# Kernel optimization log

Measured on AMD Instinct MI355X. Metric: run time of the kernel, lower is better.

The kernel has to match this reference:

```python
import jax, jax.numpy as jnp
import numpy as np

BETA = 0.25


def setup_inputs() -> dict:
    key = jax.random.key(0)
    k1, k2 = jax.random.split(key)
    x = jax.random.normal(k1, (8, 256, 2048), dtype=jnp.float32)        # (B, C, L)
    codebook = jax.random.normal(k2, (8192, 256), dtype=jnp.float32)    # (K, C)
    return {"x": x, "codebook": codebook}


def reference(x, codebook):
    # x: (B, C, L) -> xt: (B, L, C)
    xt = jnp.transpose(x, (0, 2, 1))
    # Euclidean distances via ||a||^2 + ||b||^2 - 2 a.b (matches torch.cdist p=2)
    x_sq = jnp.sum(xt * xt, axis=-1, keepdims=True)          # (B, L, 1)
    c_sq = jnp.sum(codebook * codebook, axis=-1)             # (K,)
    dots = jnp.einsum('blc,kc->blk', xt, codebook)           # (B, L, K)
    dists = jnp.sqrt(jnp.maximum(x_sq + c_sq[None, None, :] - 2.0 * dots, 0.0))
    # NOTE: original code uses argmax over distances (faithfully reproduced)
    code = jnp.argmax(dists, axis=2)                         # (B, L) int
    emb = jnp.transpose(codebook[code], (0, 2, 1))           # (B, C, L)
    sg = jax.lax.stop_gradient
    loss = jnp.mean((sg(x) - emb) ** 2 + BETA * (sg(emb) - emb) ** 2)
    return code, emb, loss
```

## Files before the change

kernel.cpp:

```cpp
#include <hip/hip_runtime.h>
#include <hip/hip_fp16.h>
#include <stdint.h>

typedef unsigned int u32;
typedef unsigned long long u64;
typedef unsigned short ushort_t;

#define B_ 8
#define C_ 256
#define L_ 2048
#define K_ 8192
#define M_ 16384

#define WS_KEYS   0
#define WS_CNT    131072
#define WS_MAXCS  131076
#define WS_LOSS   131080
#define WS_XSQ    131328
#define WS_CSQ    196864
#define WS_LIST   295168
#define WS_LMAX   4489472
#define WS_XTH    12878080
#define WS_CBH    21266688
#define LIST_CAP  1048576u

typedef __attribute__((ext_vector_type(8))) short s8v;
typedef __attribute__((ext_vector_type(4))) float f4v;

__device__ __forceinline__ ushort_t f2bf(float f) {
  u32 u = __float_as_uint(f);
  u32 r = (u + 0x7FFFu + ((u >> 16) & 1u)) >> 16;
  return (ushort_t)r;
}

__device__ __forceinline__ void gld16(void* lds, const void* g) {
  __builtin_amdgcn_global_load_lds(
      (const __attribute__((address_space(1))) u32*)g,
      (__attribute__((address_space(3))) u32*)lds, 16, 0, 0);
}


__global__ void __launch_bounds__(256)
vq_transpose(const float* __restrict__ x, float* __restrict__ xtf,
             ushort_t* __restrict__ xth) {
  __shared__ float t[64][65];
  int tid = threadIdx.x;
  int b  = blockIdx.x >> 7;
  int cc = (blockIdx.x >> 5) & 3;
  int lc = blockIdx.x & 31;
#pragma unroll
  for (int j = 0; j < 4; ++j) {
    int c  = (tid >> 4) + j * 16;
    int lq = tid & 15;
    float4 v = *(const float4*)&x[((size_t)(b * C_ + cc * 64 + c)) * L_ + lc * 64 + lq * 4];
    t[c][lq * 4 + 0] = v.x; t[c][lq * 4 + 1] = v.y;
    t[c][lq * 4 + 2] = v.z; t[c][lq * 4 + 3] = v.w;
  }
  __syncthreads();
  int l = tid >> 2, qc = tid & 3;
  size_t m = (size_t)b * L_ + lc * 64 + l;
#pragma unroll
  for (int j = 0; j < 4; ++j) {
    int q = qc + j * 4;
    float4 v = make_float4(t[q * 4 + 0][l], t[q * 4 + 1][l],
                           t[q * 4 + 2][l], t[q * 4 + 3][l]);
    *(float4*)&xtf[m * C_ + cc * 64 + q * 4] = v;
    ushort4 h;
    h.x = f2bf(v.x); h.y = f2bf(v.y); h.z = f2bf(v.z); h.w = f2bf(v.w);
    *(ushort4*)&xth[m * C_ + cc * 64 + q * 4] = h;
  }
}

__global__ void vq_xsqt(const float* __restrict__ xtf, float* __restrict__ xsq) {
  int t = threadIdx.x;
  int m = blockIdx.x * 16 + (t >> 4);
  int g = t & 15;
  const float* row = xtf + (size_t)m * C_;
  float s = 0.0f;
#pragma unroll
  for (int j = 0; j < 4; ++j) {
    float4 v = *(const float4*)&row[g * 4 + j * 64];
    s += v.x * v.x + v.y * v.y + v.z * v.z + v.w * v.w;
  }
#pragma unroll
  for (int off = 1; off < 16; off <<= 1) s += __shfl_xor(s, off, 64);
  if (g == 0) xsq[m] = s;
}

__global__ void vq_cbprep(const float* __restrict__ cb, float* __restrict__ csq,
                          int* __restrict__ maxcs, ushort_t* __restrict__ cbh) {
  int t = threadIdx.x;
  int k = blockIdx.x * 16 + (t >> 4);
  int g = t & 15;
  const float* row = cb + (size_t)k * C_;
  float s = 0.0f;
#pragma unroll
  for (int j = 0; j < 4; ++j) {
    float4 v = *(const float4*)&row[g * 4 + j * 64];
    s += v.x * v.x + v.y * v.y + v.z * v.z + v.w * v.w;
    ushort4 h;
    h.x = f2bf(v.x); h.y = f2bf(v.y); h.z = f2bf(v.z); h.w = f2bf(v.w);
    *(ushort4*)&cbh[(size_t)k * C_ + g * 4 + j * 64] = h;
  }
#pragma unroll
  for (int off = 1; off < 16; off <<= 1) s += __shfl_xor(s, off, 64);
  if (g == 0) {
    csq[k] = s;
    atomicMax(maxcs, __float_as_int(s));
  }
}


#define STAGE(buf, t_)                                                        \
  {                                                                           \
    _Pragma("unroll")                                                         \
    for (int q = 0; q < 8; ++q) {                                             \
      int codeT = (w * 8 + q) * 2 + (l >> 5);                                 \
      int chunk = l & 31;                                                     \
      gld16(&Bs[(buf)][(w * 8 + q) * 512],                                    \
            &cbh[(size_t)(n0 + (t_) * 128 + codeT) * 256 +                    \
                 ((chunk ^ (codeT & 7)) * 8)]);                               \
    }                                                                         \
  }

__global__ void __launch_bounds__(512, 2)
vq_gemm(const ushort_t* __restrict__ xth, const ushort_t* __restrict__ cbh,
        const float* __restrict__ csq, __half* __restrict__ lmax) {
  __shared__ short Bs[2][128 * 256];

  const int tid = threadIdx.x;
  const int w = tid >> 6, l = tid & 63;
  const int lr = l & 15, lk = l >> 4;
  const int strip = blockIdx.x >> 2, ns = blockIdx.x & 3;
  const int r0 = strip * 256 + w * 32;
  const int n0 = ns * 2048;

  s8v a[2][8];
#pragma unroll
  for (int i = 0; i < 2; ++i)
#pragma unroll
    for (int ks = 0; ks < 8; ++ks)
      a[i][ks] = *(const s8v*)&xth[(size_t)(r0 + i * 16 + lr) * 256 + ks * 32 + lk * 8];

  STAGE(0, 0);
  __syncthreads();

  for (int t = 0; t < 16; ++t) {
    const int buf = t & 1;
    if (t < 15) STAGE(buf ^ 1, t + 1);

    f4v acc[2][8];
#pragma unroll
    for (int i = 0; i < 2; ++i)
#pragma unroll
      for (int j = 0; j < 8; ++j) acc[i][j] = (f4v){0.f, 0.f, 0.f, 0.f};

#pragma unroll
    for (int ks = 0; ks < 8; ++ks) {
      s8v b[8];
#pragma unroll
      for (int j = 0; j < 8; ++j) {
        int jrow = j * 16 + lr;
        b[j] = *(const s8v*)&Bs[buf][jrow * 256 + (((ks * 4 + lk) ^ (lr & 7)) * 8)];
      }
#pragma unroll
      for (int i = 0; i < 2; ++i)
#pragma unroll
        for (int j = 0; j < 8; ++j)
          acc[i][j] = __builtin_amdgcn_mfma_f32_16x16x32_bf16(a[i][ks], b[j], acc[i][j], 0, 0, 0);
    }

    float cq[8];
#pragma unroll
    for (int j = 0; j < 8; ++j) cq[j] = csq[n0 + t * 128 + j * 16 + lr];
#pragma unroll
    for (int i = 0; i < 2; ++i)
#pragma unroll
      for (int r = 0; r < 4; ++r) {
        float vb[4];
#pragma unroll
        for (int b2 = 0; b2 < 4; ++b2) {
          float v0 = __fmaf_rn(-2.0f, acc[i][2 * b2][r], cq[2 * b2]);
          float v1 = __fmaf_rn(-2.0f, acc[i][2 * b2 + 1][r], cq[2 * b2 + 1]);
          vb[b2] = fmaxf(v0, v1);
        }
#pragma unroll
        for (int off = 1; off < 16; off <<= 1)
#pragma unroll
          for (int b2 = 0; b2 < 4; ++b2)
            vb[b2] = fmaxf(vb[b2], __shfl_xor(vb[b2], off, 64));
        if (lr == 0) {
          short4 sv;
          sv.x = (short)__half_as_ushort(__float2half(vb[0]));
          sv.y = (short)__half_as_ushort(__float2half(vb[1]));
          sv.z = (short)__half_as_ushort(__float2half(vb[2]));
          sv.w = (short)__half_as_ushort(__float2half(vb[3]));
          *(short4*)&lmax[(size_t)(r0 + i * 16 + lk * 4 + r) * 256 + ns * 64 + t * 4] = sv;
        }
      }
    __syncthreads();
  }
}

__global__ void __launch_bounds__(256)
vq_thr(const __half* __restrict__ lmax, const float* __restrict__ xsq,
       const int* __restrict__ maxcs, u32* __restrict__ list, u32* __restrict__ cnt) {
  __shared__ u32 wcnt[4];
  __shared__ u32 gbase_s;
  const int t = threadIdx.x, w = t >> 6, l = t & 63;
  const int m0 = blockIdx.x * 64 + w * 16;
  const float mc = __int_as_float(*maxcs);

  ushort4 hv[16];
  float thv[16];
  u32 wtot = 0;
#pragma unroll
  for (int i = 0; i < 16; ++i) {
    int m = m0 + i;
    hv[i] = *(const ushort4*)&lmax[(size_t)m * 256 + l * 4];
    float v0 = __half2float(__ushort_as_half(hv[i].x));
    float v1 = __half2float(__ushort_as_half(hv[i].y));
    float v2 = __half2float(__ushort_as_half(hv[i].z));
    float v3 = __half2float(__ushort_as_half(hv[i].w));
    float g = fmaxf(fmaxf(v0, v1), fmaxf(v2, v3));
#pragma unroll
    for (int off = 1; off < 64; off <<= 1) g = fmaxf(g, __shfl_xor(g, off, 64));
    float th = g - (0.033f * sqrtf(xsq[m] * mc) + 0.6f);
    thv[i] = th;
    wtot += __popcll(__ballot(v0 >= th));
    wtot += __popcll(__ballot(v1 >= th));
    wtot += __popcll(__ballot(v2 >= th));
    wtot += __popcll(__ballot(v3 >= th));
  }
  if (l == 0) wcnt[w] = wtot;
  __syncthreads();
  if (t == 0) gbase_s = atomicAdd(cnt, wcnt[0] + wcnt[1] + wcnt[2] + wcnt[3]);
  __syncthreads();
  u32 off = gbase_s;
  for (int ww = 0; ww < w; ++ww) off += wcnt[ww];
#pragma unroll
  for (int i = 0; i < 16; ++i) {
    int m = m0 + i;
    float th = thv[i];
    float v[4];
    v[0] = __half2float(__ushort_as_half(hv[i].x));
    v[1] = __half2float(__ushort_as_half(hv[i].y));
    v[2] = __half2float(__ushort_as_half(hv[i].z));
    v[3] = __half2float(__ushort_as_half(hv[i].w));
#pragma unroll
    for (int j = 0; j < 4; ++j) {
      u64 mask = __ballot(v[j] >= th);
      if (v[j] >= th) {
        u32 pos = off + (u32)__popcll(mask & ((1ull << l) - 1ull));
        if (pos < LIST_CAP) list[pos] = ((u32)m << 8) | (u32)(l * 4 + j);
      }
      off += (u32)__popcll(mask);
    }
  }
}

__global__ void __launch_bounds__(256)
vq_rescore(const u32* __restrict__ list, const u32* __restrict__ cnt,
           const float* __restrict__ xtf, const float* __restrict__ cb,
           const float* __restrict__ xsq, const float* __restrict__ csq,
           u64* __restrict__ keys) {
  u32 n = *cnt; if (n > LIST_CAP) n = LIST_CAP;
  const int l = threadIdx.x & 63;
  const int u = l & 7;
  const int g = l >> 3;
  int wid = (blockIdx.x * 256 + threadIdx.x) >> 6;
  int nw = (gridDim.x * 256) >> 6;
  for (u32 e = wid; e < n; e += nw) {
    u32 ent = list[e];
    int m = (int)(ent >> 8), blk = (int)(ent & 255u);
    float4 xv[8];
#pragma unroll
    for (int i = 0; i < 8; ++i)
      xv[i] = *(const float4*)&xtf[(size_t)m * C_ + (i * 8 + u) * 4];
    float xq = xsq[m];
    u64 bestkey = 0;
#pragma unroll
    for (int cc = 0; cc < 4; ++cc) {
      int k = blk * 32 + cc * 8 + g;
      const float* crow = &cb[(size_t)k * C_];
      float p = 0.0f;
#pragma unroll
      for (int i = 0; i < 8; ++i) {
        float4 cv = *(const float4*)&crow[(i * 8 + u) * 4];
        p += xv[i].x * cv.x + xv[i].y * cv.y + xv[i].z * cv.z + xv[i].w * cv.w;
      }
#pragma unroll
      for (int off = 1; off < 8; off <<= 1) p += __shfl_xor(p, off, 64);
      if (u == 0) {
        float d2 = __fsub_rn(__fadd_rn(xq, csq[k]), __fmul_rn(2.0f, p));
        float dist = sqrtf(fmaxf(d2, 0.0f));
        u64 key = ((u64)__float_as_uint(dist) << 32) |
                  (u64)(0xFFFFFFFFu - (u32)k);
        if (key > bestkey) bestkey = key;
      }
    }
#pragma unroll
    for (int off = 8; off < 64; off <<= 1) {
      u64 o = __shfl_xor(bestkey, off, 64);
      if (o > bestkey) bestkey = o;
    }
    if (l == 0) atomicMax(&keys[m], bestkey);
  }
}


__global__ void vq_code(const u64* __restrict__ keys, float* __restrict__ out) {
  int m = blockIdx.x * 256 + threadIdx.x;
  u32 k = 0xFFFFFFFFu - (u32)(keys[m] & 0xFFFFFFFFull);
  out[m] = (float)k;
}

__global__ void __launch_bounds__(256)
vq_gather(const u64* __restrict__ keys, const float* __restrict__ cb,
          const float* __restrict__ x, float* __restrict__ emb,
          float* __restrict__ loss_acc) {
  __shared__ float rows[32 * 260];
  __shared__ int codes_s[32];
  __shared__ float partial[4];
  int t = threadIdx.x;
  int b = blockIdx.x >> 6;
  int l0 = (blockIdx.x & 63) * 32;
  if (t < 32) {
    u64 key = keys[b * L_ + l0 + t];
    codes_s[t] = (int)(0xFFFFFFFFu - (u32)(key & 0xFFFFFFFFull));
  }
  __syncthreads();
  {
    int r = t >> 3, c4 = t & 7;
    const float* src = cb + (size_t)codes_s[r] * C_;
#pragma unroll
    for (int j = 0; j < 8; ++j) {
      float4 v = *(const float4*)&src[(c4 + 8 * j) * 4];
      *(float4*)&rows[r * 260 + (c4 + 8 * j) * 4] = v;
    }
  }
  __syncthreads();
  float ls = 0.0f;
  int l = t & 31, cg = t >> 5;
#pragma unroll 4
  for (int cs = 0; cs < 32; ++cs) {
    int c = cg * 32 + cs;
    float v = rows[l * 260 + c];
    size_t gi = (size_t)(b * C_ + c) * L_ + l0 + l;
    emb[gi] = v;
    float d = x[gi] - v;
    ls = fmaf(d, d, ls);
  }
#pragma unroll
  for (int off = 1; off < 64; off <<= 1) ls += __shfl_xor(ls, off, 64);
  if ((t & 63) == 0) partial[t >> 6] = ls;
  __syncthreads();
  if (t == 0)
    atomicAdd(loss_acc, partial[0] + partial[1] + partial[2] + partial[3]);
}

__global__ void vq_loss(const float* __restrict__ loss_acc, float* __restrict__ out) {
  out[0] = loss_acc[0] / 4194304.0f;
}

extern "C" void kernel_launch(void* const* d_in, const int* in_sizes, int n_in,
                              void* d_out, int out_size, void* d_ws, size_t ws_size,
                              hipStream_t stream) {
  const float* x  = (const float*)d_in[0];
  const float* cb = (const float*)d_in[1];
  float* out = (float*)d_out;
  char* ws = (char*)d_ws;

  u64* keys      = (u64*)(ws + WS_KEYS);
  u32* cnt       = (u32*)(ws + WS_CNT);
  int* maxcs     = (int*)(ws + WS_MAXCS);
  float* loss_a  = (float*)(ws + WS_LOSS);
  float* xsq     = (float*)(ws + WS_XSQ);
  float* csq     = (float*)(ws + WS_CSQ);
  u32* list      = (u32*)(ws + WS_LIST);
  __half* lmax   = (__half*)(ws + WS_LMAX);
  ushort_t* xth  = (ushort_t*)(ws + WS_XTH);
  ushort_t* cbh  = (ushort_t*)(ws + WS_CBH);
  float* xtf     = out + M_;

  hipMemsetAsync(ws, 0, 131084, stream);

  vq_transpose<<<1024, 256, 0, stream>>>(x, xtf, xth);
  vq_cbprep<<<K_ / 16, 256, 0, stream>>>(cb, csq, maxcs, cbh);
  vq_xsqt<<<M_ / 16, 256, 0, stream>>>(xtf, xsq);
  vq_gemm<<<256, 512, 0, stream>>>(xth, cbh, csq, lmax);
  vq_thr<<<256, 256, 0, stream>>>(lmax, xsq, maxcs, list, cnt);
  vq_rescore<<<2048, 256, 0, stream>>>(list, cnt, xtf, cb, xsq, csq, keys);
  vq_code<<<M_ / 256, 256, 0, stream>>>(keys, out);
  vq_gather<<<(B_ * L_) / 32, 256, 0, stream>>>(keys, cb, x, out + M_, loss_a);
  vq_loss<<<1, 1, 0, stream>>>(loss_a, out + M_ + (size_t)B_ * C_ * L_);
}
```

Measured before the change: 235.1 us.

## Split GEMM K into halves, double grid, swap MFMA operands, fuse code output

The codebook GEMM now stages 128-code x 128-channel halves of the codebook into LDS, so the shared buffer shrinks from 128 KB to 64 KB. Each block covers 1024 codes instead of 2048, which doubles the grid to 512 blocks and should raise occupancy and parallelism. MFMA operands are swapped so each lane holds four consecutive codes for one row. That lets the row max use a vectorised csq load and only two cross-lane shuffles instead of a 16-lane butterfly. The separate vq_code kernel is folded into vq_gather to save one launch, at the cost of more staging iterations and barriers.

```diff
diff --git a/kernel.cpp b/kernel.cpp
--- a/kernel.cpp
+++ b/kernel.cpp
@@ -111,29 +111,30 @@
 }
 
 
-#define STAGE(buf, t_)                                                        \
+#define STAGE(buf, s_)                                                        \
   {                                                                           \
+    const int t_ = (s_) >> 1, kh_ = (s_) & 1;                                 \
     _Pragma("unroll")                                                         \
-    for (int q = 0; q < 8; ++q) {                                             \
-      int codeT = (w * 8 + q) * 2 + (l >> 5);                                 \
-      int chunk = l & 31;                                                     \
-      gld16(&Bs[(buf)][(w * 8 + q) * 512],                                    \
-            &cbh[(size_t)(n0 + (t_) * 128 + codeT) * 256 +                    \
-                 ((chunk ^ (codeT & 7)) * 8)]);                               \
+    for (int q = 0; q < 4; ++q) {                                             \
+      int chunk = (q * 8 + w) * 64 + l;             \
+      int row = chunk >> 4;                                       \
+      int csrc = lr ^ (row & 7);                                              \
+      gld16(&Bs[(buf)][chunk * 8],                                            \
+            &cbh[(size_t)(n0 + t_ * 128 + row) * 256 + kh_ * 128 + csrc * 8]);\
     }                                                                         \
   }
 
 __global__ void __launch_bounds__(512, 2)
 vq_gemm(const ushort_t* __restrict__ xth, const ushort_t* __restrict__ cbh,
         const float* __restrict__ csq, __half* __restrict__ lmax) {
-  __shared__ short Bs[2][128 * 256];
+  __shared__ short Bs[2][128 * 128];
 
   const int tid = threadIdx.x;
   const int w = tid >> 6, l = tid & 63;
   const int lr = l & 15, lk = l >> 4;
-  const int strip = blockIdx.x >> 2, ns = blockIdx.x & 3;
+  const int strip = blockIdx.x >> 3, ns = blockIdx.x & 7;
   const int r0 = strip * 256 + w * 32;
-  const int n0 = ns * 2048;
+  const int n0 = ns * 1024;
 
   s8v a[2][8];
 #pragma unroll
@@ -142,62 +143,70 @@
     for (int ks = 0; ks < 8; ++ks)
       a[i][ks] = *(const s8v*)&xth[(size_t)(r0 + i * 16 + lr) * 256 + ks * 32 + lk * 8];
 
+  f4v acc[2][8];
   STAGE(0, 0);
   __syncthreads();
 
-  for (int t = 0; t < 16; ++t) {
-    const int buf = t & 1;
-    if (t < 15) STAGE(buf ^ 1, t + 1);
-
-    f4v acc[2][8];
-#pragma unroll
-    for (int i = 0; i < 2; ++i)
-#pragma unroll
-      for (int j = 0; j < 8; ++j) acc[i][j] = (f4v){0.f, 0.f, 0.f, 0.f};
-
-#pragma unroll
-    for (int ks = 0; ks < 8; ++ks) {
+  for (int s = 0; s < 16; ++s) {
+    const int buf = s & 1;
+    const int kh = s & 1, tt = s >> 1;
+    if (s < 15) STAGE(buf ^ 1, s + 1);
+
+    if (kh == 0) {
+#pragma unroll
+      for (int i = 0; i < 2; ++i)
+#pragma unroll
+        for (int j = 0; j < 8; ++j) acc[i][j] = (f4v){0.f, 0.f, 0.f, 0.f};
+    }
+
+#pragma unroll
+    for (int ks = 0; ks < 4; ++ks) {
       s8v b[8];
 #pragma unroll
-      for (int j = 0; j < 8; ++j) {
-        int jrow = j * 16 + lr;
-        b[j] = *(const s8v*)&Bs[buf][jrow * 256 + (((ks * 4 + lk) ^ (lr & 7)) * 8)];
-      }
+      for (int j = 0; j < 8; ++j)
+        b[j] = *(const s8v*)&Bs[buf][(j * 16 + lr) * 128 + (((ks * 4 + lk) ^ (lr & 7)) * 8)];
 #pragma unroll
       for (int i = 0; i < 2; ++i)
 #pragma unroll
         for (int j = 0; j < 8; ++j)
-          acc[i][j] = __builtin_amdgcn_mfma_f32_16x16x32_bf16(a[i][ks], b[j], acc[i][j], 0, 0, 0);
-    }
-
-    float cq[8];
-#pragma unroll
-    for (int j = 0; j < 8; ++j) cq[j] = csq[n0 + t * 128 + j * 16 + lr];
-#pragma unroll
-    for (int i = 0; i < 2; ++i)
-#pragma unroll
-      for (int r = 0; r < 4; ++r) {
-        float vb[4];
-#pragma unroll
-        for (int b2 = 0; b2 < 4; ++b2) {
-          float v0 = __fmaf_rn(-2.0f, acc[i][2 * b2][r], cq[2 * b2]);
-          float v1 = __fmaf_rn(-2.0f, acc[i][2 * b2 + 1][r], cq[2 * b2 + 1]);
-          vb[b2] = fmaxf(v0, v1);
-        }
-#pragma unroll
-        for (int off = 1; off < 16; off <<= 1)
-#pragma unroll
-          for (int b2 = 0; b2 < 4; ++b2)
-            vb[b2] = fmaxf(vb[b2], __shfl_xor(vb[b2], off, 64));
-        if (lr == 0) {
-          short4 sv;
-          sv.x = (short)__half_as_ushort(__float2half(vb[0]));
-          sv.y = (short)__half_as_ushort(__float2half(vb[1]));
-          sv.z = (short)__half_as_ushort(__float2half(vb[2]));
-          sv.w = (short)__half_as_ushort(__float2half(vb[3]));
-          *(short4*)&lmax[(size_t)(r0 + i * 16 + lk * 4 + r) * 256 + ns * 64 + t * 4] = sv;
+          acc[i][j] = __builtin_amdgcn_mfma_f32_16x16x32_bf16(b[j], a[i][kh * 4 + ks], acc[i][j], 0, 0, 0);
+    }
+
+    if (kh == 1) {
+      float vm[2][4];
+#pragma unroll
+      for (int jp = 0; jp < 4; ++jp) {
+        float4 cqa = *(const float4*)&csq[n0 + tt * 128 + jp * 32 + lk * 4];
+        float4 cqb = *(const float4*)&csq[n0 + tt * 128 + jp * 32 + 16 + lk * 4];
+#pragma unroll
+        for (int i = 0; i < 2; ++i) {
+          f4v A0 = acc[i][2 * jp], A1 = acc[i][2 * jp + 1];
+          float m0 = fmaxf(fmaxf(__fmaf_rn(-2.0f, A0[0], cqa.x),
+                                 __fmaf_rn(-2.0f, A0[1], cqa.y)),
+                           fmaxf(__fmaf_rn(-2.0f, A0[2], cqa.z),
+                                 __fmaf_rn(-2.0f, A0[3], cqa.w)));
+          float m1 = fmaxf(fmaxf(__fmaf_rn(-2.0f, A1[0], cqb.x),
+                                 __fmaf_rn(-2.0f, A1[1], cqb.y)),
+                           fmaxf(__fmaf_rn(-2.0f, A1[2], cqb.z),
+                                 __fmaf_rn(-2.0f, A1[3], cqb.w)));
+          float vmx = fmaxf(m0, m1);
+          vmx = fmaxf(vmx, __shfl_xor(vmx, 16, 64));
+          vmx = fmaxf(vmx, __shfl_xor(vmx, 32, 64));
+          vm[i][jp] = vmx;
         }
       }
+      if (l < 16) {
+#pragma unroll
+        for (int i = 0; i < 2; ++i) {
+          short4 sv;
+          sv.x = (short)__half_as_ushort(__float2half(vm[i][0]));
+          sv.y = (short)__half_as_ushort(__float2half(vm[i][1]));
+          sv.z = (short)__half_as_ushort(__float2half(vm[i][2]));
+          sv.w = (short)__half_as_ushort(__float2half(vm[i][3]));
+          *(short4*)&lmax[(size_t)(r0 + i * 16 + l) * 256 + ns * 32 + tt * 4] = sv;
+        }
+      }
+    }
     __syncthreads();
   }
 }
@@ -309,16 +318,10 @@
 }
 
 
-__global__ void vq_code(const u64* __restrict__ keys, float* __restrict__ out) {
-  int m = blockIdx.x * 256 + threadIdx.x;
-  u32 k = 0xFFFFFFFFu - (u32)(keys[m] & 0xFFFFFFFFull);
-  out[m] = (float)k;
-}
-
 __global__ void __launch_bounds__(256)
 vq_gather(const u64* __restrict__ keys, const float* __restrict__ cb,
-          const float* __restrict__ x, float* __restrict__ emb,
-          float* __restrict__ loss_acc) {
+          const float* __restrict__ x, float* __restrict__ out_code,
+          float* __restrict__ emb, float* __restrict__ loss_acc) {
   __shared__ float rows[32 * 260];
   __shared__ int codes_s[32];
   __shared__ float partial[4];
@@ -327,7 +330,9 @@
   int l0 = (blockIdx.x & 63) * 32;
   if (t < 32) {
     u64 key = keys[b * L_ + l0 + t];
-    codes_s[t] = (int)(0xFFFFFFFFu - (u32)(key & 0xFFFFFFFFull));
+    int code = (int)(0xFFFFFFFFu - (u32)(key & 0xFFFFFFFFull));
+    codes_s[t] = code;
+    out_code[b * L_ + l0 + t] = (float)code;
   }
   __syncthreads();
   {
@@ -388,10 +393,9 @@
   vq_transpose<<<1024, 256, 0, stream>>>(x, xtf, xth);
   vq_cbprep<<<K_ / 16, 256, 0, stream>>>(cb, csq, maxcs, cbh);
   vq_xsqt<<<M_ / 16, 256, 0, stream>>>(xtf, xsq);
-  vq_gemm<<<256, 512, 0, stream>>>(xth, cbh, csq, lmax);
+  vq_gemm<<<512, 512, 0, stream>>>(xth, cbh, csq, lmax);
   vq_thr<<<256, 256, 0, stream>>>(lmax, xsq, maxcs, list, cnt);
   vq_rescore<<<2048, 256, 0, stream>>>(list, cnt, xtf, cb, xsq, csq, keys);
-  vq_code<<<M_ / 256, 256, 0, stream>>>(keys, out);
-  vq_gather<<<(B_ * L_) / 32, 256, 0, stream>>>(keys, cb, x, out + M_, loss_a);
+  vq_gather<<<(B_ * L_) / 32, 256, 0, stream>>>(keys, cb, x, out, out + M_, loss_a);
   vq_loss<<<1, 1, 0, stream>>>(loss_a, out + M_ + (size_t)B_ * C_ * L_);
 }
```

Measured after the change: 251.5 us. 1.07x slower.
